# Optimization experiments

Measured on AMD Instinct MI355X. Metric: run time of the kernel, lower is better.

## Reference

```python
import jax, jax.numpy as jnp
import numpy as np
from jax import lax

B, C, H, W = 16, 256, 64, 64
KNUM, KS, STRIDE, PAD, RED, GROUPS = 4, 3, 1, 1, 16, 4
BN_EPS = 1e-5


def setup_inputs() -> dict:
    key = jax.random.key(0)
    ks = jax.random.split(key, 12)
    f = jax.random.normal
    half, red = C // 2, C // RED
    return {
        "x": f(ks[0], (B, C, H, W), jnp.float32),
        "att_conv1d_w": f(ks[1], (3,), jnp.float32) * 0.5,                      # shared Conv1d(1,1,3) in Attention
        "att_out_w": f(ks[2], (C, C), jnp.float32) * (2.0 / C) ** 0.5,          # out_channel_conv2d 1x1
        "att_kernel_w": f(ks[3], (KNUM, C), jnp.float32) * (2.0 / C) ** 0.5,    # kernel_conv2d 1x1
        "ede_weight": f(ks[4], (KNUM, C, C, KS, KS), jnp.float32) * (2.0 / (C * KS * KS)) ** 0.5,
        "lga_conv1d_w": f(ks[5], (3,), jnp.float32) * 0.5,                      # LGA Conv1d(1,1,3) with bias
        "lga_conv1d_b": f(ks[6], (1,), jnp.float32) * 0.1,
        "lga_mlp_w1": f(ks[7], (red, half), jnp.float32) * (2.0 / half) ** 0.5,  # mlp conv 1x1 (no bias)
        "lga_mlp_w2": f(ks[8], (half, red), jnp.float32) * (2.0 / red) ** 0.5,
        "bn_gamma": jnp.ones((C,), jnp.float32),
        "bn_beta": jnp.zeros((C,), jnp.float32),
    }


def _conv1d_same(v_bc, w3):
    # 1-channel cross-correlation along the channel axis, pad=1 (PyTorch Conv1d)
    y = lax.conv_general_dilated(v_bc[:, None, :], w3[None, None, :], (1,), [(1, 1)],
                                 dimension_numbers=("NCH", "OIH", "NCH"))
    return y[:, 0, :]


def reference(x, att_conv1d_w, att_out_w, att_kernel_w, ede_weight,
              lga_conv1d_w, lga_conv1d_b, lga_mlp_w1, lga_mlp_w2,
              bn_gamma, bn_beta):
    b, c, h, w = x.shape

    # ---- EDE (Q branch): dynamic per-sample conv ----
    gap = x.mean(axis=(2, 3))                              # (b, c) global avg pool
    t = _conv1d_same(gap, att_conv1d_w)                    # shared conv1d over channels
    in_att = jax.nn.sigmoid(t)[:, :, None, None]           # (b, c, 1, 1)
    out_att = jax.nn.sigmoid(t @ att_out_w.T)[:, :, None, None]
    k_att = jax.nn.softmax(t @ att_kernel_w.T, axis=1)     # (b, KNUM)
    agg_w = jnp.einsum("bk,koipq->boipq", k_att, ede_weight)  # (b, C, C, KS, KS)
    x_mod = x * in_att

    def per_sample(xi, wi):  # xi: (C,H,W), wi: (C,C,KS,KS)
        return lax.conv_general_dilated(xi[None], wi, (STRIDE, STRIDE),
                                        [(PAD, PAD), (PAD, PAD)])[0]

    Q = jax.vmap(per_sample)(x_mod, agg_w) * out_att       # (b, C, H, W)

    # ---- LGA (K branch) ----
    half = c // 2
    in1, in2 = x[:, :half], x[:, half:]
    s = _conv1d_same(in1.mean(axis=(2, 3)), lga_conv1d_w) + lga_conv1d_b
    x1 = in1 * jax.nn.sigmoid(s)[:, :, None, None]

    def mlp(v):  # (b, half) -> (b, half); 1x1 convs on (b,half,1,1) == matmuls
        return jax.nn.relu(v @ lga_mlp_w1.T) @ lga_mlp_w2.T

    ch = jax.nn.sigmoid(mlp(in2.max(axis=(2, 3))) + mlp(in2.mean(axis=(2, 3))))
    y2 = in2 * ch[:, :, None, None]
    K = jnp.concatenate([x1, y2], axis=1)
    # channel shuffle with GROUPS groups
    K = K.reshape(b, GROUPS, c // GROUPS, h, w).transpose(0, 2, 1, 3, 4).reshape(b, c, h, w)

    # ---- fuse + BatchNorm (training-mode batch stats) + ReLU ----
    z = Q + K
    mean = z.mean(axis=(0, 2, 3))
    var = z.var(axis=(0, 2, 3))
    zn = (z - mean[None, :, None, None]) * lax.rsqrt(var[None, :, None, None] + BN_EPS)
    return jax.nn.relu(zn * bn_gamma[None, :, None, None] + bn_beta[None, :, None, None])
```

## Files before the change

### kernel.cpp

```cpp
#include <hip/hip_runtime.h>
#include <hip/hip_bf16.h>
#include <stdint.h>

#define HW_ 4096

typedef float f32x4 __attribute__((ext_vector_type(4)));
typedef short bf16x8 __attribute__((ext_vector_type(8)));

__device__ __forceinline__ unsigned short f2bf(float f) {
  __hip_bfloat16 h = __float2bfloat16(f);
  return *reinterpret_cast<unsigned short*>(&h);
}
__device__ __forceinline__ float sigmoidf_(float x) { return 1.f / (1.f + __expf(-x)); }

__device__ __forceinline__ void glds16(const void* g, void* l) {
  __builtin_amdgcn_global_load_lds(
      (const __attribute__((address_space(1))) unsigned int*)g,
      (__attribute__((address_space(3))) unsigned int*)l, 16, 0, 0);
}

__global__ void k_pre(const float* __restrict__ x, unsigned short* __restrict__ xtr,
                      float* __restrict__ psum, float* __restrict__ pmax) {
  int hwb = blockIdx.x;
  int cb = blockIdx.y;
  int b = blockIdx.z;
  int t = threadIdx.x;
  __shared__ float sv[64][65];
  int h16 = t & 15, g = t >> 4;
#pragma unroll
  for (int i = 0; i < 4; ++i) {
    int c_l = g + i * 16;
    float4 v = *reinterpret_cast<const float4*>(
        x + (((size_t)b * 256 + cb * 64 + c_l) << 12) + hwb * 64 + h16 * 4);
    *reinterpret_cast<float4*>(&sv[c_l][h16 * 4]) = v;
  }
  __syncthreads();
  {
    int c_l = t >> 2, q = t & 3;
    float s16 = 0.f, m16 = -3.4e38f;
#pragma unroll
    for (int j = 0; j < 16; ++j) {
      float vv = sv[c_l][q * 16 + j];
      s16 += vv; m16 = fmaxf(m16, vv);
    }
    s16 += __shfl_xor(s16, 1); s16 += __shfl_xor(s16, 2);
    m16 = fmaxf(m16, __shfl_xor(m16, 1)); m16 = fmaxf(m16, __shfl_xor(m16, 2));
    if (q == 0) {
      int c = cb * 64 + c_l;
      psum[(((size_t)b * 256 + c) << 6) + hwb] = s16;
      pmax[(((size_t)b * 256 + c) << 6) + hwb] = m16;
    }
  }
#pragma unroll
  for (int i = 0; i < 2; ++i) {
    int fp = t + i * 256;
    int hw2 = fp >> 3;
    int cp = (fp & 7) * 8;
    uint4 uu;
    uu.x = (unsigned)f2bf(sv[cp + 0][hw2]) | ((unsigned)f2bf(sv[cp + 1][hw2]) << 16);
    uu.y = (unsigned)f2bf(sv[cp + 2][hw2]) | ((unsigned)f2bf(sv[cp + 3][hw2]) << 16);
    uu.z = (unsigned)f2bf(sv[cp + 4][hw2]) | ((unsigned)f2bf(sv[cp + 5][hw2]) << 16);
    uu.w = (unsigned)f2bf(sv[cp + 6][hw2]) | ((unsigned)f2bf(sv[cp + 7][hw2]) << 16);
    *reinterpret_cast<uint4*>(xtr + (((size_t)b * 4096 + hwb * 64 + hw2) << 8) + cb * 64 + cp) = uu;
  }
}

__global__ void k_tiny(const float* __restrict__ psum, const float* __restrict__ pmax,
                       const float* __restrict__ aw3, const float* __restrict__ Wout,
                       const float* __restrict__ Wk, const float* __restrict__ lw3,
                       const float* __restrict__ lbia, const float* __restrict__ mw1,
                       const float* __restrict__ mw2,
                       float* __restrict__ in_att, float* __restrict__ out_att,
                       float* __restrict__ katt, float* __restrict__ sc,
                       float* __restrict__ sums, float* __restrict__ zerop) {
  int b = blockIdx.x, t = threadIdx.x;
  __shared__ float g[256], tt[256], red[256], hsum[16], ksm[4], mx[128];
  {
    const float4* pp = reinterpret_cast<const float4*>(psum + ((size_t)(b * 256 + t) << 6));
    const float4* pm = reinterpret_cast<const float4*>(pmax + ((size_t)(b * 256 + t) << 6));
    float s = 0.f, m = -3.4e38f;
#pragma unroll
    for (int j = 0; j < 16; ++j) {
      float4 a = pp[j]; s += (a.x + a.y) + (a.z + a.w);
      float4 q4 = pm[j];
      m = fmaxf(m, fmaxf(fmaxf(q4.x, q4.y), fmaxf(q4.z, q4.w)));
    }
    g[t] = s * (1.f / 4096.f);
    if (t >= 128) mx[t - 128] = m;
  }
  if (b == 0) {
    sums[t] = 0.f; sums[256 + t] = 0.f;
    zerop[t] = 0.f;
  }
  __syncthreads();
  float c0 = aw3[0], c1 = aw3[1], c2 = aw3[2];
  float tv = c1 * g[t];
  if (t > 0) tv += c0 * g[t - 1];
  if (t < 255) tv += c2 * g[t + 1];
  tt[t] = tv;
  in_att[b * 256 + t] = sigmoidf_(tv);
  __syncthreads();
  {
    float d = 0.f;
    const float4* wr = reinterpret_cast<const float4*>(Wout + (size_t)t * 256);
    for (int c4 = 0; c4 < 64; ++c4) {
      float4 wv4 = wr[c4];
      d += tt[c4 * 4] * wv4.x + tt[c4 * 4 + 1] * wv4.y + tt[c4 * 4 + 2] * wv4.z + tt[c4 * 4 + 3] * wv4.w;
    }
    out_att[b * 256 + t] = sigmoidf_(d);
  }
  int k = t >> 6, lane = t & 63;
  {
    float pk = 0.f;
    for (int c = lane; c < 256; c += 64) pk += tt[c] * Wk[k * 256 + c];
    red[t] = pk; __syncthreads();
    for (int off = 32; off > 0; off >>= 1) {
      if (lane < off) red[t] += red[t + off];
      __syncthreads();
    }
    if (t == 0) {
      float l0 = red[0], l1 = red[64], l2 = red[128], l3 = red[192];
      float mm = fmaxf(fmaxf(l0, l1), fmaxf(l2, l3));
      float e0 = __expf(l0 - mm), e1 = __expf(l1 - mm), e2 = __expf(l2 - mm), e3 = __expf(l3 - mm);
      float inv = 1.f / (e0 + e1 + e2 + e3);
      ksm[0] = e0 * inv; ksm[1] = e1 * inv; ksm[2] = e2 * inv; ksm[3] = e3 * inv;
    }
    __syncthreads();
    if (t < 4) katt[b * 4 + t] = ksm[t];
  }
  if (t < 128) {
    float a0 = lw3[0], a1 = lw3[1], a2 = lw3[2];
    float sv = a1 * g[t] + lbia[0];
    if (t > 0) sv += a0 * g[t - 1];
    if (t < 127) sv += a2 * g[t + 1];
    sc[b * 256 + t] = sigmoidf_(sv);
  }
  __syncthreads();
  if (t < 16) {
    float d1 = 0.f, d2 = 0.f;
    const float* w1r = mw1 + t * 128;
    for (int j = 0; j < 128; ++j) { d1 += mx[j] * w1r[j]; d2 += g[128 + j] * w1r[j]; }
    hsum[t] = fmaxf(d1, 0.f) + fmaxf(d2, 0.f);
  }
  __syncthreads();
  if (t < 128) {
    float dd = 0.f;
    const float* w2r = mw2 + t * 16;
    for (int r = 0; r < 16; ++r) dd += hsum[r] * w2r[r];
    sc[b * 256 + 128 + t] = sigmoidf_(dd);
  }
}

__global__ __launch_bounds__(256) void k_agg(const float* __restrict__ ede,
                                             const float* __restrict__ katt,
                                             const float* __restrict__ inatt,
                                             unsigned short* __restrict__ agg) {
  __shared__ float eds[4][2304];
  int o = blockIdx.x, t = threadIdx.x;
#pragma unroll
  for (int k = 0; k < 4; ++k) {
    const float* src = ede + ((size_t)k * 256 + o) * 2304;
#pragma unroll
    for (int j = 0; j < 9; ++j) eds[k][j * 256 + t] = src[j * 256 + t];
  }
  __syncthreads();
  int ii = (t & 127) * 2;
  int bh = t >> 7;
  for (int b2 = 0; b2 < 8; ++b2) {
    int b = b2 * 2 + bh;
    float k0 = katt[b * 4], k1 = katt[b * 4 + 1], k2 = katt[b * 4 + 2], k3 = katt[b * 4 + 3];
    float ia0 = inatt[b * 256 + ii], ia1 = inatt[b * 256 + ii + 1];
    size_t obase = ((size_t)(b * 256 + o) * 9) << 8;
#pragma unroll
    for (int pq = 0; pq < 9; ++pq) {
      float v0 = k0 * eds[0][ii * 9 + pq] + k1 * eds[1][ii * 9 + pq] +
                 k2 * eds[2][ii * 9 + pq] + k3 * eds[3][ii * 9 + pq];
      float v1 = k0 * eds[0][(ii + 1) * 9 + pq] + k1 * eds[1][(ii + 1) * 9 + pq] +
                 k2 * eds[2][(ii + 1) * 9 + pq] + k3 * eds[3][(ii + 1) * 9 + pq];
      v0 *= ia0; v1 *= ia1;
      unsigned int u = (unsigned)f2bf(v0) | ((unsigned)f2bf(v1) << 16);
      *reinterpret_cast<unsigned int*>(agg + obase + (pq << 8) + ii) = u;
    }
  }
}

__global__ __launch_bounds__(512, 2) void k_conv(
    const unsigned short* __restrict__ agg, const unsigned short* __restrict__ xtr,
    const float* __restrict__ x, const float* __restrict__ oatt,
    const float* __restrict__ sc, const float* __restrict__ zerop,
    float* __restrict__ sums, float* __restrict__ zout) {
  __shared__ __align__(16) char smem[114688];
  int wg = blockIdx.x;
  int bswz = ((wg & 7) << 5) | (wg >> 3);
  int b = bswz >> 4, pt = bswz & 15;
  int tid = threadIdx.x;
  int l = tid & 63;
  int wv = tid >> 6;
  int wm = wv >> 2, wn = wv & 3;
  int w0 = l & 15, ks = l >> 4;
  bool maskl0 = (w0 == 0), maskl15 = (w0 == 15);

  int r0 = tid >> 2, s0 = tid & 3;
  int r1 = r0 + 128;
  int f0 = (s0 ^ ((r0 >> 1) & 3)) << 3;
  int f1 = (s0 ^ ((r1 >> 1) & 3)) << 3;
  const unsigned short* aS0 = agg + (size_t)(b * 256 + r0) * 2304 + f0;
  const unsigned short* aS1 = agg + (size_t)(b * 256 + r1) * 2304 + f1;

  auto slabsrc = [&](int j) -> const char* {
    int idx = j * 512 + tid;
    int P = idx >> 2, sp = idx & 3;
    int sr = P >> 6, w = P & 63;
    int imgrow = pt * 4 + sr - 1;
    int ir = imgrow < 0 ? 0 : (imgrow > 63 ? 63 : imgrow);
    int slog = sp ^ ((w >> 1) & 3);
    const char* gp = (const char*)(xtr + (((size_t)b * 4096 + ir * 64 + w) << 8) + slog * 8);
    return ((unsigned)imgrow < 64u) ? gp : (const char*)zerop;
  };
  const char* sb0_ = slabsrc(0);
  const char* sb1_ = slabsrc(1);
  const char* sb2_ = slabsrc(2);

  int aOff[8];
#pragma unroll
  for (int fm = 0; fm < 8; ++fm) {
    int R = wm * 128 + fm * 16 + (l & 15);
    aOff[fm] = R * 64 + (((l >> 4) ^ ((R >> 1) & 3)) << 4);
  }

  f32x4 acc[8][4];
  f32x4 zero4 = {0.f, 0.f, 0.f, 0.f};
#pragma unroll
  for (int i2 = 0; i2 < 8; ++i2)
#pragma unroll
    for (int j2 = 0; j2 < 4; ++j2) acc[i2][j2] = zero4;

  bf16x8 z8 = {0, 0, 0, 0, 0, 0, 0, 0};

#define ASTG(COLELEMS, DSTIDX)                                           \
  { char* ad_ = smem + (DSTIDX) * 16384;                                 \
    glds16(aS0 + (COLELEMS), ad_ + tid * 16);                            \
    glds16(aS1 + (COLELEMS), ad_ + 8192 + tid * 16); }

#define SLSTG(CN)                                                        \
  { char* sd_ = smem + 65536 + (((CN) & 1) ? 24576 : 0);                 \
    glds16(sb0_ + (CN) * 64, sd_ + tid * 16);                            \
    glds16(sb1_ + (CN) * 64, sd_ + 8192 + tid * 16);                     \
    glds16(sb2_ + (CN) * 64, sd_ + 16384 + tid * 16); }

#define CITER(PQ, STG, VM)                                               \
  {                                                                      \
    __builtin_amdgcn_s_barrier();                                        \
    STG;                                                                 \
    asm volatile("s_waitcnt vmcnt(" VM ")" ::: "memory");                \
    const char* ab_ = smem + ((c + (PQ)) & 3) * 16384;                   \
    bf16x8 af_[8], bv_[4];                                               \
    _Pragma("unroll")                                                    \
    for (int f_ = 0; f_ < 8; ++f_)                                       \
      af_[f_] = *reinterpret_cast<const bf16x8*>(ab_ + aOff[f_]);        \
    const int dq_ = (PQ) % 3;                                            \
    const int rowb_ = (wn + (PQ) / 3) << 6;                              \
    _Pragma("unroll")                                                    \
    for (int fn_ = 0; fn_ < 4; ++fn_) {                                  \
      int wcol_ = w0 + fn_ * 16 + (dq_ - 1);                             \
      int wc_ = wcol_ < 0 ? 0 : (wcol_ > 63 ? 63 : wcol_);               \
      int bo_ = ((rowb_ + wc_) << 6) + ((ks ^ ((wc_ >> 1) & 3)) << 4);   \
      bv_[fn_] = *reinterpret_cast<const bf16x8*>(sb + bo_);             \
    }                                                                    \
    if (dq_ == 0) bv_[0] = maskl0 ? z8 : bv_[0];                         \
    if (dq_ == 2) bv_[3] = maskl15 ? z8 : bv_[3];                        \
    __builtin_amdgcn_s_setprio(1);                                       \
    _Pragma("unroll")                                                    \
    for (int fm_ = 0; fm_ < 8; ++fm_)                                    \
      _Pragma("unroll")                                                  \
      for (int fn_ = 0; fn_ < 4; ++fn_)                                  \
        acc[fm_][fn_] = __builtin_amdgcn_mfma_f32_16x16x32_bf16(         \
            af_[fm_], bv_[fn_], acc[fm_][fn_], 0, 0, 0);                 \
    __builtin_amdgcn_s_setprio(0);                                       \
  }

  SLSTG(0);
  ASTG(0, 0);
  ASTG(256, 1);
  ASTG(512, 2);
  asm volatile("s_waitcnt vmcnt(4)" ::: "memory");

  for (int c = 0; c < 7; ++c) {
    const char* sb = smem + 65536 + ((c & 1) ? 24576 : 0);
    CITER(0, { SLSTG(c + 1); ASTG(3 * 256 + c * 32, (c + 3) & 3); }, "7")
    CITER(1, ASTG(4 * 256 + c * 32, (c + 4) & 3), "7")
    CITER(2, ASTG(5 * 256 + c * 32, (c + 5) & 3), "4")
    CITER(3, ASTG(6 * 256 + c * 32, (c + 6) & 3), "4")
    CITER(4, ASTG(7 * 256 + c * 32, (c + 7) & 3), "4")
    CITER(5, ASTG(8 * 256 + c * 32, (c + 8) & 3), "4")
    CITER(6, ASTG(0 * 256 + (c + 1) * 32, (c + 9) & 3), "4")
    CITER(7, ASTG(1 * 256 + (c + 1) * 32, (c + 10) & 3), "4")
    CITER(8, ASTG(2 * 256 + (c + 1) * 32, (c + 11) & 3), "4")
  }
  {
    const int c = 7;
    const char* sb = smem + 65536 + 24576;
    CITER(0, ASTG(3 * 256 + 224, 2), "4")
    CITER(1, ASTG(4 * 256 + 224, 3), "4")
    CITER(2, ASTG(5 * 256 + 224, 0), "4")
    CITER(3, ASTG(6 * 256 + 224, 1), "4")
    CITER(4, ASTG(7 * 256 + 224, 2), "4")
    CITER(5, ASTG(8 * 256 + 224, 3), "4")
    CITER(6, {}, "2")
    CITER(7, {}, "0")
    CITER(8, {}, "0")
  }
#undef CITER
#undef ASTG
#undef SLSTG
  __syncthreads();

  float* ls = (float*)smem;
  ls[tid] = 0.f;
  __syncthreads();

#pragma unroll
  for (int fm = 0; fm < 8; ++fm) {
#pragma unroll
    for (int r = 0; r < 4; ++r) {
      int m = wm * 128 + fm * 16 + ((l >> 4) << 2) + r;
      int oc = ((m & 3) << 6) | (m >> 2);
      float oav = oatt[b * 256 + m];
      float scv = sc[b * 256 + oc];
      const float* xrow = x + (((size_t)b * 256 + oc) << 12) + pt * 256;
      float* zrow = zout + (((size_t)b * 256 + m) << 12) + pt * 256;
      float psv = 0.f, psv2 = 0.f;
#pragma unroll
      for (int fn = 0; fn < 4; ++fn) {
        int n = wn * 64 + fn * 16 + (l & 15);
        float zv = acc[fm][fn][r] * oav + xrow[n] * scv;
        zrow[n] = zv;
        psv += zv; psv2 += zv * zv;
      }
#pragma unroll
      for (int d = 8; d > 0; d >>= 1) {
        psv += __shfl_down(psv, d, 16);
        psv2 += __shfl_down(psv2, d, 16);
      }
      if ((l & 15) == 0) {
        atomicAdd(&ls[m], psv);
        atomicAdd(&ls[256 + m], psv2);
      }
    }
  }
  __syncthreads();
  if (tid < 256) {
    atomicAdd(&sums[tid], ls[tid]);
    atomicAdd(&sums[256 + tid], ls[256 + tid]);
  }
}

__global__ void k_apply(float* __restrict__ z, const float* __restrict__ sums,
                        const float* __restrict__ gamma, const float* __restrict__ beta) {
  int idx = blockIdx.x * 256 + threadIdx.x;
  for (int i = idx; i < 4194304; i += 4096 * 256) {
    int c = (i >> 10) & 255;
    float mean = sums[c] * (1.f / 65536.f);
    float var = sums[256 + c] * (1.f / 65536.f) - mean * mean;
    float scale = gamma[c] * rsqrtf(var + 1e-5f);
    float shift = beta[c] - mean * scale;
    float4* p = reinterpret_cast<float4*>(z) + i;
    float4 v = *p;
    v.x = fmaxf(v.x * scale + shift, 0.f);
    v.y = fmaxf(v.y * scale + shift, 0.f);
    v.z = fmaxf(v.z * scale + shift, 0.f);
    v.w = fmaxf(v.w * scale + shift, 0.f);
    *p = v;
  }
}

extern "C" void kernel_launch(void* const* d_in, const int* in_sizes, int n_in,
                              void* d_out, int out_size, void* d_ws, size_t ws_size,
                              hipStream_t stream) {
  (void)in_sizes; (void)n_in; (void)out_size; (void)ws_size;
  const float* x = (const float*)d_in[0];
  const float* aw3 = (const float*)d_in[1];
  const float* Wout = (const float*)d_in[2];
  const float* Wk = (const float*)d_in[3];
  const float* ede = (const float*)d_in[4];
  const float* lw3 = (const float*)d_in[5];
  const float* lbia = (const float*)d_in[6];
  const float* mw1 = (const float*)d_in[7];
  const float* mw2 = (const float*)d_in[8];
  const float* gamma = (const float*)d_in[9];
  const float* beta = (const float*)d_in[10];

  char* ws = (char*)d_ws;
  float* inatt = (float*)(ws + 32768);
  float* oatt  = (float*)(ws + 49152);
  float* katt  = (float*)(ws + 65536);
  float* sc    = (float*)(ws + 65792);
  float* zerop = (float*)(ws + 82176);
  float* sums  = (float*)(ws + 83200);
  unsigned short* xtr = (unsigned short*)(ws + 262144);
  unsigned short* agg = (unsigned short*)(ws + 262144 + 33554432);
  float* psum = (float*)(ws + 262144 + 33554432);
  float* pmax = (float*)(ws + 262144 + 33554432 + 1048576);
  float* z = (float*)d_out;

  k_pre<<<dim3(64, 4, 16), 256, 0, stream>>>(x, xtr, psum, pmax);
  k_tiny<<<16, 256, 0, stream>>>(psum, pmax, aw3, Wout, Wk, lw3, lbia, mw1, mw2,
                                 inatt, oatt, katt, sc, sums, zerop);
  k_agg<<<256, 256, 0, stream>>>(ede, katt, inatt, agg);
  k_conv<<<256, 512, 0, stream>>>(agg, xtr, x, oatt, sc, zerop, sums, z);
  k_apply<<<4096, 256, 0, stream>>>(z, sums, gamma, beta);
}
```

Measured before the change: 148.8 us.

## Double-buffer three conv taps per stage to cut barriers in k_conv

Replaces the 4-slot single-tap A-operand ring, which had one barrier and a staged async load per tap, with a double buffer. Each buffer holds the three horizontal taps of one kernel row, so each barrier now covers three taps of MFMA work while the next row's weights load in the background. LDS use grows to 144 KB per block to hold the two 48 KB A buffers plus the slab double buffer. Each phase ends with a full vmcnt(0) wait, so any load latency not hidden behind the three taps of compute will stall the waves.

```diff
diff --git a/kernel.cpp b/kernel.cpp
--- a/kernel.cpp
+++ b/kernel.cpp
@@ -189,7 +189,7 @@
     const float* __restrict__ x, const float* __restrict__ oatt,
     const float* __restrict__ sc, const float* __restrict__ zerop,
     float* __restrict__ sums, float* __restrict__ zout) {
-  __shared__ __align__(16) char smem[114688];
+  __shared__ __align__(16) char smem[147456];
   int wg = blockIdx.x;
   int bswz = ((wg & 7) << 5) | (wg >> 3);
   int b = bswz >> 4, pt = bswz & 15;
@@ -237,82 +237,71 @@
 
   bf16x8 z8 = {0, 0, 0, 0, 0, 0, 0, 0};
 
-#define ASTG(COLELEMS, DSTIDX)                                           \
-  { char* ad_ = smem + (DSTIDX) * 16384;                                 \
-    glds16(aS0 + (COLELEMS), ad_ + tid * 16);                            \
-    glds16(aS1 + (COLELEMS), ad_ + 8192 + tid * 16); }
-
-#define SLSTG(CN)                                                        \
-  { char* sd_ = smem + 65536 + (((CN) & 1) ? 24576 : 0);                 \
-    glds16(sb0_ + (CN) * 64, sd_ + tid * 16);                            \
-    glds16(sb1_ + (CN) * 64, sd_ + 8192 + tid * 16);                     \
-    glds16(sb2_ + (CN) * 64, sd_ + 16384 + tid * 16); }
-
-#define CITER(PQ, STG, VM)                                               \
-  {                                                                      \
-    __builtin_amdgcn_s_barrier();                                        \
-    STG;                                                                 \
-    asm volatile("s_waitcnt vmcnt(" VM ")" ::: "memory");                \
-    const char* ab_ = smem + ((c + (PQ)) & 3) * 16384;                   \
-    bf16x8 af_[8], bv_[4];                                               \
-    _Pragma("unroll")                                                    \
-    for (int f_ = 0; f_ < 8; ++f_)                                       \
-      af_[f_] = *reinterpret_cast<const bf16x8*>(ab_ + aOff[f_]);        \
-    const int dq_ = (PQ) % 3;                                            \
-    const int rowb_ = (wn + (PQ) / 3) << 6;                              \
-    _Pragma("unroll")                                                    \
-    for (int fn_ = 0; fn_ < 4; ++fn_) {                                  \
-      int wcol_ = w0 + fn_ * 16 + (dq_ - 1);                             \
-      int wc_ = wcol_ < 0 ? 0 : (wcol_ > 63 ? 63 : wcol_);               \
-      int bo_ = ((rowb_ + wc_) << 6) + ((ks ^ ((wc_ >> 1) & 3)) << 4);   \
-      bv_[fn_] = *reinterpret_cast<const bf16x8*>(sb + bo_);             \
-    }                                                                    \
-    if (dq_ == 0) bv_[0] = maskl0 ? z8 : bv_[0];                         \
-    if (dq_ == 2) bv_[3] = maskl15 ? z8 : bv_[3];                        \
-    __builtin_amdgcn_s_setprio(1);                                       \
-    _Pragma("unroll")                                                    \
-    for (int fm_ = 0; fm_ < 8; ++fm_)                                    \
-      _Pragma("unroll")                                                  \
-      for (int fn_ = 0; fn_ < 4; ++fn_)                                  \
-        acc[fm_][fn_] = __builtin_amdgcn_mfma_f32_16x16x32_bf16(         \
-            af_[fm_], bv_[fn_], acc[fm_][fn_], 0, 0, 0);                 \
-    __builtin_amdgcn_s_setprio(0);                                       \
-  }
-
-  SLSTG(0);
-  ASTG(0, 0);
-  ASTG(256, 1);
-  ASTG(512, 2);
-  asm volatile("s_waitcnt vmcnt(4)" ::: "memory");
-
-  for (int c = 0; c < 7; ++c) {
-    const char* sb = smem + 65536 + ((c & 1) ? 24576 : 0);
-    CITER(0, { SLSTG(c + 1); ASTG(3 * 256 + c * 32, (c + 3) & 3); }, "7")
-    CITER(1, ASTG(4 * 256 + c * 32, (c + 4) & 3), "7")
-    CITER(2, ASTG(5 * 256 + c * 32, (c + 5) & 3), "4")
-    CITER(3, ASTG(6 * 256 + c * 32, (c + 6) & 3), "4")
-    CITER(4, ASTG(7 * 256 + c * 32, (c + 7) & 3), "4")
-    CITER(5, ASTG(8 * 256 + c * 32, (c + 8) & 3), "4")
-    CITER(6, ASTG(0 * 256 + (c + 1) * 32, (c + 9) & 3), "4")
-    CITER(7, ASTG(1 * 256 + (c + 1) * 32, (c + 10) & 3), "4")
-    CITER(8, ASTG(2 * 256 + (c + 1) * 32, (c + 11) & 3), "4")
-  }
   {
-    const int c = 7;
-    const char* sb = smem + 65536 + 24576;
-    CITER(0, ASTG(3 * 256 + 224, 2), "4")
-    CITER(1, ASTG(4 * 256 + 224, 3), "4")
-    CITER(2, ASTG(5 * 256 + 224, 0), "4")
-    CITER(3, ASTG(6 * 256 + 224, 1), "4")
-    CITER(4, ASTG(7 * 256 + 224, 2), "4")
-    CITER(5, ASTG(8 * 256 + 224, 3), "4")
-    CITER(6, {}, "2")
-    CITER(7, {}, "0")
-    CITER(8, {}, "0")
-  }
-#undef CITER
-#undef ASTG
-#undef SLSTG
+    char* sd = smem + 98304;
+    glds16(sb0_, sd + tid * 16);
+    glds16(sb1_, sd + 8192 + tid * 16);
+    glds16(sb2_, sd + 16384 + tid * 16);
+    char* ar = smem;
+#pragma unroll
+    for (int dq = 0; dq < 3; ++dq) {
+      glds16(aS0 + dq * 256, ar + dq * 16384 + tid * 16);
+      glds16(aS1 + dq * 256, ar + dq * 16384 + 8192 + tid * 16);
+    }
+  }
+  asm volatile("s_waitcnt vmcnt(0)" ::: "memory");
+  __builtin_amdgcn_s_barrier();
+
+  int ph = 0;
+  for (int c = 0; c < 8; ++c) {
+    const char* sb = smem + 98304 + ((c & 1) ? 24576 : 0);
+    for (int dp = 0; dp < 3; ++dp, ++ph) {
+      if (ph < 23) {
+        int nc = (dp == 2) ? c + 1 : c;
+        int ndp = (dp == 2) ? 0 : dp + 1;
+        char* ar = smem + ((ph + 1) & 1) * 49152;
+#pragma unroll
+        for (int dq = 0; dq < 3; ++dq) {
+          int cols = (ndp * 3 + dq) * 256 + nc * 32;
+          glds16(aS0 + cols, ar + dq * 16384 + tid * 16);
+          glds16(aS1 + cols, ar + dq * 16384 + 8192 + tid * 16);
+        }
+      }
+      if (dp == 2 && c < 7) {
+        char* sd = smem + 98304 + (((c + 1) & 1) ? 24576 : 0);
+        glds16(sb0_ + (c + 1) * 64, sd + tid * 16);
+        glds16(sb1_ + (c + 1) * 64, sd + 8192 + tid * 16);
+        glds16(sb2_ + (c + 1) * 64, sd + 16384 + tid * 16);
+      }
+      const char* abase = smem + (ph & 1) * 49152;
+      int rowb = (wn + dp) << 6;
+#pragma unroll
+      for (int dq = 0; dq < 3; ++dq) {
+        const char* ab = abase + dq * 16384;
+        bf16x8 af[8], bv[4];
+#pragma unroll
+        for (int f = 0; f < 8; ++f) af[f] = *reinterpret_cast<const bf16x8*>(ab + aOff[f]);
+#pragma unroll
+        for (int fn = 0; fn < 4; ++fn) {
+          int wcol = w0 + fn * 16 + (dq - 1);
+          int wc = wcol < 0 ? 0 : (wcol > 63 ? 63 : wcol);
+          int bo = ((rowb + wc) << 6) + ((ks ^ ((wc >> 1) & 3)) << 4);
+          bv[fn] = *reinterpret_cast<const bf16x8*>(sb + bo);
+        }
+        if (dq == 0) bv[0] = maskl0 ? z8 : bv[0];
+        if (dq == 2) bv[3] = maskl15 ? z8 : bv[3];
+        __builtin_amdgcn_s_setprio(1);
+#pragma unroll
+        for (int fm = 0; fm < 8; ++fm)
+#pragma unroll
+          for (int fn = 0; fn < 4; ++fn)
+            acc[fm][fn] = __builtin_amdgcn_mfma_f32_16x16x32_bf16(af[fm], bv[fn], acc[fm][fn], 0, 0, 0);
+        __builtin_amdgcn_s_setprio(0);
+      }
+      asm volatile("s_waitcnt vmcnt(0)" ::: "memory");
+      __builtin_amdgcn_s_barrier();
+    }
+  }
   __syncthreads();
 
   float* ls = (float*)smem;
```

Result: no change. 148.9 us, median of 2 (+0.1%).

## Restructure conv main loop into two-phase ping-pong with double-buffered A tiles

Applied to the files above, without the earlier changes.

Replaces the 4-deep A-tile ring and vmcnt-based prefetch with a double-buffered A tile and a per-tap schedule. Each tap now loads half the A fragments, issues the next global->LDS prefetch, runs 16 MFMAs, then loads the second half and runs 16 more, with explicit barriers, lgkmcnt/vmcnt(0) waits and sched_barriers between phases. LDS drops from 112KB to 80KB, which could allow higher occupancy and lowers register pressure for A fragments. The cost is a shorter prefetch distance (only one tap ahead, waiting vmcnt(0) every tap) and four barriers per tap, which can expose global latency.

```diff
diff --git a/kernel.cpp b/kernel.cpp
--- a/kernel.cpp
+++ b/kernel.cpp
@@ -189,7 +189,7 @@
     const float* __restrict__ x, const float* __restrict__ oatt,
     const float* __restrict__ sc, const float* __restrict__ zerop,
     float* __restrict__ sums, float* __restrict__ zout) {
-  __shared__ __align__(16) char smem[114688];
+  __shared__ __align__(16) char smem[81920];
   int wg = blockIdx.x;
   int bswz = ((wg & 7) << 5) | (wg >> 3);
   int b = bswz >> 4, pt = bswz & 15;
@@ -237,80 +237,90 @@
 
   bf16x8 z8 = {0, 0, 0, 0, 0, 0, 0, 0};
 
-#define ASTG(COLELEMS, DSTIDX)                                           \
-  { char* ad_ = smem + (DSTIDX) * 16384;                                 \
-    glds16(aS0 + (COLELEMS), ad_ + tid * 16);                            \
-    glds16(aS1 + (COLELEMS), ad_ + 8192 + tid * 16); }
+#define ASTG(NPQ, NC, NT)                                                \
+  { char* ad_ = smem + 49152 + ((NT) & 1) * 16384;                       \
+    glds16(aS0 + (NPQ) * 256 + (NC) * 32, ad_ + tid * 16);               \
+    glds16(aS1 + (NPQ) * 256 + (NC) * 32, ad_ + 8192 + tid * 16); }
 
 #define SLSTG(CN)                                                        \
-  { char* sd_ = smem + 65536 + (((CN) & 1) ? 24576 : 0);                 \
+  { char* sd_ = smem + (((CN) & 1) ? 24576 : 0);                         \
     glds16(sb0_ + (CN) * 64, sd_ + tid * 16);                            \
     glds16(sb1_ + (CN) * 64, sd_ + 8192 + tid * 16);                     \
     glds16(sb2_ + (CN) * 64, sd_ + 16384 + tid * 16); }
 
-#define CITER(PQ, STG, VM)                                               \
+#define TAP(T, PQ, C, DOA, DOSLAB, NPQ, NC)                              \
   {                                                                      \
+    const char* ab_ = smem + 49152 + ((T) & 1) * 16384;                  \
+    const char* sb_ = smem + (((C) & 1) ? 24576 : 0);                    \
+    bf16x8 af_[4], bv_[4];                                               \
+    _Pragma("unroll")                                                    \
+    for (int f_ = 0; f_ < 4; ++f_)                                       \
+      af_[f_] = *reinterpret_cast<const bf16x8*>(ab_ + aOff[f_]);        \
+    {                                                                    \
+      const int dq_ = (PQ) % 3;                                          \
+      const int rowb_ = (wn + (PQ) / 3) << 6;                            \
+      _Pragma("unroll")                                                  \
+      for (int fn_ = 0; fn_ < 4; ++fn_) {                                \
+        int wcol_ = w0 + fn_ * 16 + (dq_ - 1);                           \
+        int wc_ = wcol_ < 0 ? 0 : (wcol_ > 63 ? 63 : wcol_);             \
+        int bo_ = ((rowb_ + wc_) << 6) + ((ks ^ ((wc_ >> 1) & 3)) << 4); \
+        bv_[fn_] = *reinterpret_cast<const bf16x8*>(sb_ + bo_);          \
+      }                                                                  \
+      if (dq_ == 0) bv_[0] = maskl0 ? z8 : bv_[0];                       \
+      if (dq_ == 2) bv_[3] = maskl15 ? z8 : bv_[3];                      \
+    }                                                                    \
+    if (DOA) ASTG(NPQ, NC, (T) + 1);                                     \
+    if (DOSLAB) SLSTG((C) + 1);                                          \
     __builtin_amdgcn_s_barrier();                                        \
-    STG;                                                                 \
-    asm volatile("s_waitcnt vmcnt(" VM ")" ::: "memory");                \
-    const char* ab_ = smem + ((c + (PQ)) & 3) * 16384;                   \
-    bf16x8 af_[8], bv_[4];                                               \
-    _Pragma("unroll")                                                    \
-    for (int f_ = 0; f_ < 8; ++f_)                                       \
-      af_[f_] = *reinterpret_cast<const bf16x8*>(ab_ + aOff[f_]);        \
-    const int dq_ = (PQ) % 3;                                            \
-    const int rowb_ = (wn + (PQ) / 3) << 6;                              \
-    _Pragma("unroll")                                                    \
-    for (int fn_ = 0; fn_ < 4; ++fn_) {                                  \
-      int wcol_ = w0 + fn_ * 16 + (dq_ - 1);                             \
-      int wc_ = wcol_ < 0 ? 0 : (wcol_ > 63 ? 63 : wcol_);               \
-      int bo_ = ((rowb_ + wc_) << 6) + ((ks ^ ((wc_ >> 1) & 3)) << 4);   \
-      bv_[fn_] = *reinterpret_cast<const bf16x8*>(sb + bo_);             \
-    }                                                                    \
-    if (dq_ == 0) bv_[0] = maskl0 ? z8 : bv_[0];                         \
-    if (dq_ == 2) bv_[3] = maskl15 ? z8 : bv_[3];                        \
+    asm volatile("s_waitcnt lgkmcnt(0)" ::: "memory");                   \
+    __builtin_amdgcn_sched_barrier(0);                                   \
     __builtin_amdgcn_s_setprio(1);                                       \
     _Pragma("unroll")                                                    \
-    for (int fm_ = 0; fm_ < 8; ++fm_)                                    \
+    for (int fm_ = 0; fm_ < 4; ++fm_)                                    \
       _Pragma("unroll")                                                  \
       for (int fn_ = 0; fn_ < 4; ++fn_)                                  \
         acc[fm_][fn_] = __builtin_amdgcn_mfma_f32_16x16x32_bf16(         \
             af_[fm_], bv_[fn_], acc[fm_][fn_], 0, 0, 0);                 \
     __builtin_amdgcn_s_setprio(0);                                       \
+    __builtin_amdgcn_sched_barrier(0);                                   \
+    __builtin_amdgcn_s_barrier();                                        \
+    bf16x8 ag_[4];                                                       \
+    _Pragma("unroll")                                                    \
+    for (int f_ = 0; f_ < 4; ++f_)                                       \
+      ag_[f_] = *reinterpret_cast<const bf16x8*>(ab_ + aOff[4 + f_]);    \
+    __builtin_amdgcn_s_barrier();                                        \
+    asm volatile("s_waitcnt lgkmcnt(0)" ::: "memory");                   \
+    __builtin_amdgcn_sched_barrier(0);                                   \
+    __builtin_amdgcn_s_setprio(1);                                       \
+    _Pragma("unroll")                                                    \
+    for (int fm_ = 0; fm_ < 4; ++fm_)                                    \
+      _Pragma("unroll")                                                  \
+      for (int fn_ = 0; fn_ < 4; ++fn_)                                  \
+        acc[4 + fm_][fn_] = __builtin_amdgcn_mfma_f32_16x16x32_bf16(     \
+            ag_[fm_], bv_[fn_], acc[4 + fm_][fn_], 0, 0, 0);             \
+    __builtin_amdgcn_s_setprio(0);                                       \
+    __builtin_amdgcn_sched_barrier(0);                                   \
+    asm volatile("s_waitcnt vmcnt(0)" ::: "memory");                     \
+    __builtin_amdgcn_s_barrier();                                        \
   }
 
   SLSTG(0);
-  ASTG(0, 0);
-  ASTG(256, 1);
-  ASTG(512, 2);
-  asm volatile("s_waitcnt vmcnt(4)" ::: "memory");
-
-  for (int c = 0; c < 7; ++c) {
-    const char* sb = smem + 65536 + ((c & 1) ? 24576 : 0);
-    CITER(0, { SLSTG(c + 1); ASTG(3 * 256 + c * 32, (c + 3) & 3); }, "7")
-    CITER(1, ASTG(4 * 256 + c * 32, (c + 4) & 3), "7")
-    CITER(2, ASTG(5 * 256 + c * 32, (c + 5) & 3), "4")
-    CITER(3, ASTG(6 * 256 + c * 32, (c + 6) & 3), "4")
-    CITER(4, ASTG(7 * 256 + c * 32, (c + 7) & 3), "4")
-    CITER(5, ASTG(8 * 256 + c * 32, (c + 8) & 3), "4")
-    CITER(6, ASTG(0 * 256 + (c + 1) * 32, (c + 9) & 3), "4")
-    CITER(7, ASTG(1 * 256 + (c + 1) * 32, (c + 10) & 3), "4")
-    CITER(8, ASTG(2 * 256 + (c + 1) * 32, (c + 11) & 3), "4")
-  }
-  {
-    const int c = 7;
-    const char* sb = smem + 65536 + 24576;
-    CITER(0, ASTG(3 * 256 + 224, 2), "4")
-    CITER(1, ASTG(4 * 256 + 224, 3), "4")
-    CITER(2, ASTG(5 * 256 + 224, 0), "4")
-    CITER(3, ASTG(6 * 256 + 224, 1), "4")
-    CITER(4, ASTG(7 * 256 + 224, 2), "4")
-    CITER(5, ASTG(8 * 256 + 224, 3), "4")
-    CITER(6, {}, "2")
-    CITER(7, {}, "0")
-    CITER(8, {}, "0")
-  }
-#undef CITER
+  ASTG(0, 0, 0);
+  asm volatile("s_waitcnt vmcnt(0)" ::: "memory");
+  __builtin_amdgcn_s_barrier();
+
+  for (int c = 0; c < 8; ++c) {
+#pragma unroll
+    for (int pq = 0; pq < 9; ++pq) {
+      int t = c * 9 + pq;
+      int npq = (pq < 8) ? pq + 1 : 0;
+      int nc = (pq < 8) ? c : c + 1;
+      bool doA = (t < 71);
+      bool doSlab = (pq == 0) && (c < 7);
+      TAP(t, pq, c, doA, doSlab, npq, nc)
+    }
+  }
+#undef TAP
 #undef ASTG
 #undef SLSTG
   __syncthreads();
```

Measured after the change: 150.0 us. About the same (+0.8%).
